# Optimization experiments

Measured on AMD Instinct MI355X. Metric: run time of the kernel, lower is better.

## Reference

```python
import jax, jax.numpy as jnp
import numpy as np

B, S, D_MODEL, N_HEADS = 2, 2048, 2048, 16
HEAD_DIM = D_MODEL // N_HEADS
SCALE = 1.0 / np.sqrt(HEAD_DIM)
SOFTCAP = 30.0
NEG = -10000.0


def _apply_rope(h):
    # h: [B, S, H, D]; faithful to torch ref: repeat_interleave'd cos/sin with
    # half-split rotate_half.
    seq, d = h.shape[1], h.shape[3]
    pos = jnp.arange(seq, dtype=jnp.float32)
    inv_freq = 1.0 / (10000.0 ** (jnp.arange(0, d, 2, dtype=jnp.float32) / d))
    phase = pos[:, None] * inv_freq[None, :]                      # [S, D/2]
    cos = jnp.repeat(jnp.cos(phase), 2, axis=-1)[None, :, None, :].astype(h.dtype)
    sin = jnp.repeat(jnp.sin(phase), 2, axis=-1)[None, :, None, :].astype(h.dtype)
    rot = jnp.concatenate([-h[..., d // 2:], h[..., :d // 2]], axis=-1)
    return h * cos + rot * sin


def setup_inputs() -> dict:
    key = jax.random.key(0)
    k1, k2, k3, k4, k5 = jax.random.split(key, 5)
    hidden_states = jax.random.normal(k1, (B, S, D_MODEL), dtype=jnp.float32)
    # causal allowed-attention mask [S, S]; True = attention permitted
    allowed_attention = jnp.tril(jnp.ones((S, S), dtype=bool))
    # no padding (True would mean padded position)
    padding_mask = jnp.zeros((B, S), dtype=bool)
    std = 1.0 / np.sqrt(D_MODEL)
    Wq = jax.random.normal(k2, (D_MODEL, D_MODEL), dtype=jnp.float32) * std
    Wk = jax.random.normal(k3, (D_MODEL, D_MODEL), dtype=jnp.float32) * std
    Wv = jax.random.normal(k4, (D_MODEL, D_MODEL), dtype=jnp.float32) * std
    Wo = jax.random.normal(k5, (D_MODEL, D_MODEL), dtype=jnp.float32) * std
    return {"hidden_states": hidden_states, "allowed_attention": allowed_attention,
            "padding_mask": padding_mask, "Wq": Wq, "Wk": Wk, "Wv": Wv, "Wo": Wo}


def reference(hidden_states, allowed_attention, padding_mask, Wq, Wk, Wv, Wo):
    b, s, _ = hidden_states.shape
    q = (hidden_states @ Wq.T).reshape(b, s, N_HEADS, HEAD_DIM)
    k = (hidden_states @ Wk.T).reshape(b, s, N_HEADS, HEAD_DIM)
    v = (hidden_states @ Wv.T).reshape(b, s, N_HEADS, HEAD_DIM)
    q = _apply_rope(q)
    k = _apply_rope(k)
    logits = jnp.einsum('bthd,bshd->bhts', q, k).astype(jnp.float32) * SCALE
    logits = SOFTCAP * jnp.tanh(logits / SOFTCAP)
    logits = jnp.where(allowed_attention[None, None, :, :], logits, NEG)
    logits = jnp.where(padding_mask[:, None, None, :], NEG, logits)
    weights = jax.nn.softmax(logits, axis=-1).astype(q.dtype)
    attended = jnp.einsum('bhts,bshd->bthd', weights, v).reshape(b, s, D_MODEL)
    out = attended @ Wo.T
    return jnp.where(padding_mask[:, :, None], 0.0, out)
```

## Files before the change

kernel.cpp:

```cpp
#include <hip/hip_runtime.h>
#include <hip/hip_bf16.h>

#define S_LEN 2048
#define NH    16
#define HD    128
#define BHN   32
#define DM    2048
#define MTOK  4096
#define NTK   32

typedef __attribute__((ext_vector_type(8))) short short8;
typedef __attribute__((ext_vector_type(4))) float f32x4;

__device__ __forceinline__ unsigned short f2bf(float x){
  union { __hip_bfloat16 h; unsigned short u; } c; c.h = __float2bfloat16(x); return c.u;
}
__device__ __forceinline__ float bf2f(unsigned short u){
  union { unsigned short u; __hip_bfloat16 h; } c; c.u = u; return __bfloat162float(c.h);
}

__global__ void cvt_kernel(const float* __restrict__ src, unsigned short* __restrict__ dst, int n4){
  int i = blockIdx.x*256 + threadIdx.x;
  if (i >= n4) return;
  float4 v = reinterpret_cast<const float4*>(src)[i];
  ushort4 o;
  o.x = f2bf(v.x); o.y = f2bf(v.y); o.z = f2bf(v.z); o.w = f2bf(v.w);
  reinterpret_cast<ushort4*>(dst)[i] = o;
}

__global__ void cvt_w_kernel(const float* __restrict__ s0, const float* __restrict__ s1,
                             const float* __restrict__ s2, const float* __restrict__ s3,
                             unsigned short* __restrict__ dqkv, unsigned short* __restrict__ dwo,
                             int n4each){
  int which = blockIdx.y;
  const float* src = (which==0) ? s0 : (which==1) ? s1 : (which==2) ? s2 : s3;
  unsigned short* dst = (which<3) ? (dqkv + (size_t)which*DM*DM) : dwo;
  int i = blockIdx.x*256 + threadIdx.x;
  if (i >= n4each) return;
  float4 v = reinterpret_cast<const float4*>(src)[i];
  ushort4 o;
  o.x = f2bf(v.x); o.y = f2bf(v.y); o.z = f2bf(v.z); o.w = f2bf(v.w);
  reinterpret_cast<ushort4*>(dst)[i] = o;
}

__global__ void rope_table_kernel(float* __restrict__ cosT, float* __restrict__ sinT){
  int s = blockIdx.x, i = threadIdx.x;
  float inv = powf(10000.f, -(float)i * (1.f/64.f));
  float ph = (float)s * inv;
  float sv, cv; sincosf(ph, &sv, &cv);
  cosT[s*64 + i] = cv; sinT[s*64 + i] = sv;
}

__global__ void rope_apply2_kernel(unsigned short* __restrict__ Q, unsigned short* __restrict__ K,
                                   const float* __restrict__ cosT, const float* __restrict__ sinT){
  int gid = blockIdx.x*256 + threadIdx.x;
  unsigned short* X = (gid < (BHN*S_LEN*64)) ? Q : K;
  int g = gid & (BHN*S_LEN*64 - 1);
  int j = g & 63, row = g >> 6, s = row & (S_LEN-1);
  unsigned short* p = X + (size_t)row*HD;
  float h0 = bf2f(p[j]), h1 = bf2f(p[j+64]);
  int f0 = j >> 1;
  float c0 = cosT[s*64+f0],    s0 = sinT[s*64+f0];
  float c1 = cosT[s*64+32+f0], s1 = sinT[s*64+32+f0];
  p[j]    = f2bf(h0*c0 - h1*s0);
  p[j+64] = f2bf(h1*c1 + h0*s1);
}

#define MFMA8(ACC) \
  __builtin_amdgcn_s_setprio(1); \
  _Pragma("unroll") \
  for (int mi=0;mi<4;++mi){ \
    ACC[mi] = __builtin_amdgcn_mfma_f32_16x16x32_bf16(af[mi*2+0], bf[0], ACC[mi], 0,0,0); \
    ACC[mi] = __builtin_amdgcn_mfma_f32_16x16x32_bf16(af[mi*2+1], bf[1], ACC[mi], 0,0,0); \
  } \
  __builtin_amdgcn_s_setprio(0);

template<int MODE>
__global__ __launch_bounds__(512)
void gemm_8p(const unsigned short* __restrict__ A, const unsigned short* __restrict__ B,
             float* __restrict__ C0, unsigned short* __restrict__ Cq,
             unsigned short* __restrict__ Ck, unsigned short* __restrict__ Cv){
  extern __shared__ unsigned char sm[];
  const int t = threadIdx.x;
  const int lane = t & 63, w = t >> 6;
  const int lr = lane & 15, lg = lane >> 4;
  const int wm = w >> 2, wn = w & 3;
  int id = blockIdx.x, bm, bn;
  if (MODE == 3){ int swz = (id & 7)*96 + (id >> 3); bm = swz/48; bn = swz%48; }
  else          { int swz = (id & 7)*32 + (id >> 3); bm = swz/16; bn = swz%16; }
  const size_t rs = 4096;
  const unsigned char* Ab = (const unsigned char*)A + (size_t)bm*256*rs;
  const unsigned char* Bb = (const unsigned char*)B + (size_t)bn*128*rs;
  const int r0 = t >> 3, c0 = t & 7;

  auto stage = [&](int tkt, int slot){
    if (tkt >= NTK) return;
    unsigned char* hb = sm + ((tkt & 1) ? 49152 : 0);
    if (slot < 2){
      const unsigned char* sb = Ab + (size_t)(slot ? 128 : 0)*rs + (size_t)tkt*128;
      hb += slot*16384;
      __builtin_amdgcn_global_load_lds(
          (const unsigned int*)(sb + (size_t)r0*rs + ((unsigned)(c0 ^ (r0 & 7)) << 4)),
          (unsigned int*)(hb + t*16), 16, 0, 0);
      int r1 = r0 + 64;
      __builtin_amdgcn_global_load_lds(
          (const unsigned int*)(sb + (size_t)r1*rs + ((unsigned)(c0 ^ (r1 & 7)) << 4)),
          (unsigned int*)(hb + 8192 + t*16), 16, 0, 0);
    } else {
      const unsigned char* sb = Bb + (size_t)((slot-2) ? 64 : 0)*rs + (size_t)tkt*128;
      hb += 32768 + (slot-2)*8192;
      __builtin_amdgcn_global_load_lds(
          (const unsigned int*)(sb + (size_t)r0*rs + ((unsigned)(c0 ^ (r0 & 7)) << 4)),
          (unsigned int*)(hb + t*16), 16, 0, 0);
    }
  };

  short8 af[8], bf[2];
  auto loadA = [&](int d, int rh){
#pragma unroll
    for (int mi=0;mi<4;++mi){
      int row = wm*64 + mi*16 + lr;
      const unsigned char* rp = sm + d*49152 + rh*16384 + row*128;
      int x = row & 7;
      af[mi*2+0] = *reinterpret_cast<const short8*>(rp + (((0+lg) ^ x) << 4));
      af[mi*2+1] = *reinterpret_cast<const short8*>(rp + (((4+lg) ^ x) << 4));
    }
  };
  auto loadB = [&](int d, int ch){
    int row = wn*16 + lr;
    const unsigned char* rp = sm + d*49152 + 32768 + ch*8192 + row*128;
    int x = row & 7;
    bf[0] = *reinterpret_cast<const short8*>(rp + (((0+lg) ^ x) << 4));
    bf[1] = *reinterpret_cast<const short8*>(rp + (((4+lg) ^ x) << 4));
  };

  f32x4 acc00[4] = {}, acc01[4] = {}, acc11[4] = {}, acc10[4] = {};

  stage(0,0); stage(0,2); stage(0,3); stage(0,1);
  stage(1,0); stage(1,3); stage(1,1);
  asm volatile("s_waitcnt vmcnt(5)" ::: "memory");
  __builtin_amdgcn_s_barrier();

  for (int g = 0; g < NTK; ++g){
    const int d = g & 1;
    loadA(d, 0); loadB(d, 0);
    stage(g+1, 2);
    __builtin_amdgcn_s_barrier();
    MFMA8(acc00);
    __builtin_amdgcn_s_barrier();
    loadB(d, 1);
    stage(g+2, 0);
    __builtin_amdgcn_s_barrier();
    MFMA8(acc01);
    __builtin_amdgcn_s_barrier();
    loadA(d, 1);
    stage(g+2, 3);
    __builtin_amdgcn_s_barrier();
    MFMA8(acc11);
    __builtin_amdgcn_s_barrier();
    loadB(d, 0);
    stage(g+2, 1);
    __builtin_amdgcn_s_barrier();
    MFMA8(acc10);
    if (g < NTK-1){
      if (g == NTK-2) { asm volatile("s_waitcnt vmcnt(0)" ::: "memory"); }
      else            { asm volatile("s_waitcnt vmcnt(5)" ::: "memory"); }
    }
    __builtin_amdgcn_s_barrier();
  }

  auto epi = [&](const f32x4* acc, int rh, int ch){
#pragma unroll
    for (int mi=0;mi<4;++mi){
      int col  = bn*128 + ch*64 + wn*16 + lr;
      int rowb = bm*256 + rh*128 + wm*64 + mi*16 + lg*4;
      if (MODE == 0){
#pragma unroll
        for (int rr=0;rr<4;++rr)
          C0[(size_t)(rowb+rr)*DM + col] = acc[mi][rr];
      } else {
        if (col < 4096){
          unsigned short* dst = (col < 2048) ? Cq : Ck;
          int cc = col & 2047, h = cc >> 7, dd = cc & 127;
#pragma unroll
          for (int rr=0;rr<4;++rr){
            int row = rowb + rr, bb = row >> 11, s = row & 2047;
            dst[(((size_t)(bb*16+h)*2048 + s)<<7) + dd] = f2bf(acc[mi][rr]);
          }
        } else {
          int cc = col - 4096, h = cc >> 7, dd = cc & 127;
          ushort4 pk;
          pk.x = f2bf(acc[mi][0]); pk.y = f2bf(acc[mi][1]);
          pk.z = f2bf(acc[mi][2]); pk.w = f2bf(acc[mi][3]);
          int bb = rowb >> 11, s = rowb & 2047, kb = s >> 6, kvl = s & 63;
          *reinterpret_cast<ushort4*>(&Cv[(((size_t)((bb*16+h)*32 + kb)*128 + dd)<<6) + kvl]) = pk;
        }
      }
    }
  };
  epi(acc00,0,0); epi(acc01,0,1); epi(acc11,1,1); epi(acc10,1,0);
}

__global__ __launch_bounds__(256, 2)
void attn_kernel(const unsigned short* __restrict__ Qr, const unsigned short* __restrict__ Kr,
                 const unsigned short* __restrict__ Vp, unsigned short* __restrict__ AO){
  const int bid = blockIdx.x;
  const int qb  = (bid < 256) ? (15 - (bid >> 5)) : ((bid >> 5) - 8);
  const int bh  = bid & 31;
  const int t = threadIdx.x;
  const int w = t >> 6, lane = t & 63, lr = lane & 15, lg = lane >> 4;
  const int qbase = qb*128 + w*32;
  const int diag_w = (qbase + 31) >> 6;
  const int kmax = qb*2 + 1;
  const unsigned short* Qh = Qr + (size_t)bh*S_LEN*HD;
  const unsigned char*  Kg = (const unsigned char*)(Kr + (size_t)bh*S_LEN*HD);
  const unsigned char*  Vg = (const unsigned char*)Vp + (size_t)bh*32*16384;

  __shared__ __align__(16) unsigned short Ks[8192];
  __shared__ __align__(16) unsigned short Vs[8192];
  __shared__ __align__(16) unsigned short Ps[4][32][72];

  short8 qa[2][4];
#pragma unroll
  for (int f=0;f<2;++f)
#pragma unroll
    for (int kc=0;kc<4;++kc)
      qa[f][kc] = *reinterpret_cast<const short8*>(&Qh[(size_t)(qbase + f*16 + lr)*HD + kc*32 + lg*8]);

  float lsum[2] = {0.f, 0.f};
  f32x4 o[2][8] = {};

  const float C1 = 2.f * 0.08838834764831845f * 1.4426950408889634f / 30.f;
  const float C2 = -60.f * 1.4426950408889634f;

  for (int kb = 0; kb <= kmax; ++kb){
    const unsigned char* Kt = Kg + (size_t)kb*(64*256);
    const unsigned char* Vt = Vg + (size_t)kb*16384;
#pragma unroll
    for (int j=0;j<4;++j){
      unsigned int L  = (unsigned int)(w*4+j)*1024u + (unsigned int)lane*16u;
      unsigned int rK = L >> 8;
      unsigned int sK = (L & 255u) ^ ((rK & 15u) << 4);
      __builtin_amdgcn_global_load_lds((const unsigned int*)(Kt + (rK<<8) + sK),
          (unsigned int*)((unsigned char*)Ks + (size_t)(w*4+j)*1024), 16, 0, 0);
      unsigned int rV = L >> 7;
      unsigned int sV = (L & 127u) ^ ((rV & 7u) << 4);
      __builtin_amdgcn_global_load_lds((const unsigned int*)(Vt + (rV<<7) + sV),
          (unsigned int*)((unsigned char*)Vs + (size_t)(w*4+j)*1024), 16, 0, 0);
    }
    __syncthreads();
    if (kb <= diag_w){
      f32x4 s[2][4] = {};
      __builtin_amdgcn_s_setprio(1);
#pragma unroll
      for (int nf=0;nf<4;++nf)
#pragma unroll
        for (int kc=0;kc<4;++kc){
          unsigned int byt = ((unsigned int)(nf*16+lr) << 8) + (((unsigned int)(kc*64 + lg*16)) ^ ((unsigned int)(lr&15) << 4));
          short8 kf = *reinterpret_cast<const short8*>((const unsigned char*)Ks + byt);
          s[0][nf] = __builtin_amdgcn_mfma_f32_16x16x32_bf16(kf, qa[0][kc], s[0][nf], 0,0,0);
          s[1][nf] = __builtin_amdgcn_mfma_f32_16x16x32_bf16(kf, qa[1][kc], s[1][nf], 0,0,0);
        }
      __builtin_amdgcn_s_setprio(0);
#pragma unroll
      for (int f=0;f<2;++f){
#pragma unroll
        for (int nf=0;nf<4;++nf){
#pragma unroll
          for (int r=0;r<4;++r){
            float u = __builtin_amdgcn_exp2f(s[f][nf][r] * C1);
            float p = __builtin_amdgcn_exp2f(C2 * __builtin_amdgcn_rcpf(u + 1.f));
            if (kb == diag_w){
              int kvi = kb*64 + nf*16 + lg*4 + r;
              if (kvi > qbase + f*16 + lr) p = 0.f;
            }
            s[f][nf][r] = p;
            lsum[f] += p;
          }
          ushort4 pk;
          pk.x = f2bf(s[f][nf][0]); pk.y = f2bf(s[f][nf][1]);
          pk.z = f2bf(s[f][nf][2]); pk.w = f2bf(s[f][nf][3]);
          *reinterpret_cast<ushort4*>(&Ps[w][f*16+lr][nf*16 + lg*4]) = pk;
        }
      }
      short8 pb[2][2];
#pragma unroll
      for (int f=0;f<2;++f)
#pragma unroll
        for (int kc2=0;kc2<2;++kc2)
          pb[f][kc2] = *reinterpret_cast<const short8*>(&Ps[w][f*16+lr][kc2*32 + lg*8]);
      __builtin_amdgcn_s_setprio(1);
#pragma unroll
      for (int df=0;df<8;++df)
#pragma unroll
        for (int kc2=0;kc2<2;++kc2){
          unsigned int byt = ((unsigned int)(df*16+lr) << 7) + (((unsigned int)(kc2*64 + lg*16)) ^ ((unsigned int)(lr&7) << 4));
          short8 vb = *reinterpret_cast<const short8*>((const unsigned char*)Vs + byt);
          o[0][df] = __builtin_amdgcn_mfma_f32_16x16x32_bf16(vb, pb[0][kc2], o[0][df], 0,0,0);
          o[1][df] = __builtin_amdgcn_mfma_f32_16x16x32_bf16(vb, pb[1][kc2], o[1][df], 0,0,0);
        }
      __builtin_amdgcn_s_setprio(0);
    }
    __syncthreads();
  }
#pragma unroll
  for (int f=0;f<2;++f){
    lsum[f] += __shfl_xor(lsum[f], 16);
    lsum[f] += __shfl_xor(lsum[f], 32);
  }
  const int bb = bh >> 4, h = bh & 15;
#pragma unroll
  for (int f=0;f<2;++f){
    const float inv = 1.f / lsum[f];
    const int qi = qbase + f*16 + lr;
#pragma unroll
    for (int df=0;df<8;++df){
      ushort4 pk;
      pk.x = f2bf(o[f][df][0] * inv); pk.y = f2bf(o[f][df][1] * inv);
      pk.z = f2bf(o[f][df][2] * inv); pk.w = f2bf(o[f][df][3] * inv);
      *reinterpret_cast<ushort4*>(&AO[((size_t)(bb*S_LEN + qi))*DM + h*HD + df*16 + lg*4]) = pk;
    }
  }
}

extern "C" void kernel_launch(void* const* d_in, const int* in_sizes, int n_in,
                              void* d_out, int out_size, void* d_ws, size_t ws_size,
                              hipStream_t stream){
  const float* hs = (const float*)d_in[0];
  const float* Wq = (const float*)d_in[3];
  const float* Wk = (const float*)d_in[4];
  const float* Wv = (const float*)d_in[5];
  const float* Wo = (const float*)d_in[6];

  uint8_t* base = (uint8_t*)d_ws;
  unsigned short* hsb  = (unsigned short*)base; base += (size_t)MTOK*DM*2;
  unsigned short* wqkv = (unsigned short*)base; base += (size_t)3*DM*DM*2;
  unsigned short* wob  = (unsigned short*)base; base += (size_t)DM*DM*2;
  unsigned short* Qr   = (unsigned short*)base; base += (size_t)MTOK*DM*2;
  unsigned short* Kr   = (unsigned short*)base; base += (size_t)MTOK*DM*2;
  unsigned short* Vp   = (unsigned short*)base; base += (size_t)MTOK*DM*2;
  unsigned short* AO   = (unsigned short*)base; base += (size_t)MTOK*DM*2;
  float* cosT = (float*)base;                   base += (size_t)S_LEN*64*4;
  float* sinT = (float*)base;                   base += (size_t)S_LEN*64*4;

  cvt_kernel<<<(MTOK*DM/4)/256, 256, 0, stream>>>(hs, hsb, MTOK*DM/4);
  cvt_w_kernel<<<dim3((DM*DM/4)/256, 4), 256, 0, stream>>>(Wq, Wk, Wv, Wo, wqkv, wob, DM*DM/4);
  rope_table_kernel<<<S_LEN, 64, 0, stream>>>(cosT, sinT);

  hipFuncSetAttribute((const void*)gemm_8p<3>,
                      hipFuncAttributeMaxDynamicSharedMemorySize, 98304);
  hipFuncSetAttribute((const void*)gemm_8p<0>,
                      hipFuncAttributeMaxDynamicSharedMemorySize, 98304);

  gemm_8p<3><<<768, 512, 98304, stream>>>(hsb, wqkv, nullptr, Qr, Kr, Vp);

  rope_apply2_kernel<<<(2*BHN*S_LEN*64)/256, 256, 0, stream>>>(Qr, Kr, cosT, sinT);

  attn_kernel<<<512, 256, 0, stream>>>(Qr, Kr, Vp, AO);

  gemm_8p<0><<<256, 512, 98304, stream>>>(AO, wob, (float*)d_out, nullptr, nullptr, nullptr);
}
```

Before: 285.1 us.

## Replace 8-phase GEMM with two-phase double-buffered GEMM using wider N tiles

Replaces the 8-phase ping-pong GEMM (256x128 tiles, four sub-phase barriers per k-step) with a simpler two-phase loop. Each k-step prefetches the whole next tile into the other buffer, then runs all MFMAs for the current one. Tiles become 128x384 for the QKV projection (512 blocks, 128KB LDS) and 128x256 for the output projection. The block-to-tile mapping changes to a new swizzle. The aim is fewer barriers and more MFMA work per LDS fill, at the cost of a full vmcnt(0) wait each iteration, more registers for larger accumulators, and possibly lower occupancy.

After: 267.2 us. 1.07x faster.

```diff
diff --git a/kernel.cpp b/kernel.cpp
--- a/kernel.cpp
+++ b/kernel.cpp
@@ -66,118 +66,97 @@
   p[j+64] = f2bf(h1*c1 + h0*s1);
 }
 
-#define MFMA8(ACC) \
-  __builtin_amdgcn_s_setprio(1); \
-  _Pragma("unroll") \
-  for (int mi=0;mi<4;++mi){ \
-    ACC[mi] = __builtin_amdgcn_mfma_f32_16x16x32_bf16(af[mi*2+0], bf[0], ACC[mi], 0,0,0); \
-    ACC[mi] = __builtin_amdgcn_mfma_f32_16x16x32_bf16(af[mi*2+1], bf[1], ACC[mi], 0,0,0); \
-  } \
-  __builtin_amdgcn_s_setprio(0);
-
 template<int MODE>
 __global__ __launch_bounds__(512)
-void gemm_8p(const unsigned short* __restrict__ A, const unsigned short* __restrict__ B,
-             float* __restrict__ C0, unsigned short* __restrict__ Cq,
-             unsigned short* __restrict__ Ck, unsigned short* __restrict__ Cv){
+void gemm_2ph(const unsigned short* __restrict__ A, const unsigned short* __restrict__ B,
+              float* __restrict__ C0, unsigned short* __restrict__ Cq,
+              unsigned short* __restrict__ Ck, unsigned short* __restrict__ Cv){
+  constexpr int BN   = (MODE==3) ? 384 : 256;
+  constexpr int NJ   = BN/64;
+  constexpr int NBJ  = BN/64;
+  constexpr int BUFSZ = 16384 + BN*128;
   extern __shared__ unsigned char sm[];
   const int t = threadIdx.x;
   const int lane = t & 63, w = t >> 6;
   const int lr = lane & 15, lg = lane >> 4;
   const int wm = w >> 2, wn = w & 3;
-  int id = blockIdx.x, bm, bn;
-  if (MODE == 3){ int swz = (id & 7)*96 + (id >> 3); bm = swz/48; bn = swz%48; }
-  else          { int swz = (id & 7)*32 + (id >> 3); bm = swz/16; bn = swz%16; }
+  int bm, bn;
+  if (MODE == 3){ int x = blockIdx.x & 7, i = blockIdx.x >> 3;
+                  bn = x*2 + (i >> 5); bm = i & 31; }
+  else          { bn = blockIdx.x & 7; bm = blockIdx.x >> 3; }
   const size_t rs = 4096;
-  const unsigned char* Ab = (const unsigned char*)A + (size_t)bm*256*rs;
-  const unsigned char* Bb = (const unsigned char*)B + (size_t)bn*128*rs;
+  const unsigned char* Ab = (const unsigned char*)A + (size_t)bm*128*rs;
+  const unsigned char* Bb = (const unsigned char*)B + (size_t)bn*BN*rs;
   const int r0 = t >> 3, c0 = t & 7;
-
-  auto stage = [&](int tkt, int slot){
+  const int cs = (c0 ^ (r0 & 7)) << 4;
+
+  auto stage = [&](int tkt){
     if (tkt >= NTK) return;
-    unsigned char* hb = sm + ((tkt & 1) ? 49152 : 0);
-    if (slot < 2){
-      const unsigned char* sb = Ab + (size_t)(slot ? 128 : 0)*rs + (size_t)tkt*128;
-      hb += slot*16384;
-      __builtin_amdgcn_global_load_lds(
-          (const unsigned int*)(sb + (size_t)r0*rs + ((unsigned)(c0 ^ (r0 & 7)) << 4)),
-          (unsigned int*)(hb + t*16), 16, 0, 0);
-      int r1 = r0 + 64;
-      __builtin_amdgcn_global_load_lds(
-          (const unsigned int*)(sb + (size_t)r1*rs + ((unsigned)(c0 ^ (r1 & 7)) << 4)),
-          (unsigned int*)(hb + 8192 + t*16), 16, 0, 0);
-    } else {
-      const unsigned char* sb = Bb + (size_t)((slot-2) ? 64 : 0)*rs + (size_t)tkt*128;
-      hb += 32768 + (slot-2)*8192;
-      __builtin_amdgcn_global_load_lds(
-          (const unsigned int*)(sb + (size_t)r0*rs + ((unsigned)(c0 ^ (r0 & 7)) << 4)),
-          (unsigned int*)(hb + t*16), 16, 0, 0);
-    }
+    unsigned char* hb = sm + (tkt & 1)*BUFSZ;
+    const unsigned char* At = Ab + (size_t)tkt*128;
+    __builtin_amdgcn_global_load_lds((const unsigned int*)(At + (size_t)r0*rs + cs),
+        (unsigned int*)(hb + t*16), 16, 0, 0);
+    __builtin_amdgcn_global_load_lds((const unsigned int*)(At + (size_t)(r0+64)*rs + cs),
+        (unsigned int*)(hb + 8192 + t*16), 16, 0, 0);
+    const unsigned char* Bt = Bb + (size_t)tkt*128;
+#pragma unroll
+    for (int j=0;j<NBJ;++j)
+      __builtin_amdgcn_global_load_lds((const unsigned int*)(Bt + (size_t)(r0+64*j)*rs + cs),
+          (unsigned int*)(hb + 16384 + (size_t)(t + 512*j)*16), 16, 0, 0);
   };
 
-  short8 af[8], bf[2];
-  auto loadA = [&](int d, int rh){
+  f32x4 acc[4][NJ] = {};
+
+  stage(0);
+  asm volatile("s_waitcnt vmcnt(0)" ::: "memory");
+  __builtin_amdgcn_s_barrier();
+
+  for (int g = 0; g < NTK; ++g){
+    stage(g+1);
+    const unsigned char* hb = sm + (g & 1)*BUFSZ;
+    short8 af[8];
 #pragma unroll
     for (int mi=0;mi<4;++mi){
       int row = wm*64 + mi*16 + lr;
-      const unsigned char* rp = sm + d*49152 + rh*16384 + row*128;
-      int x = row & 7;
-      af[mi*2+0] = *reinterpret_cast<const short8*>(rp + (((0+lg) ^ x) << 4));
-      af[mi*2+1] = *reinterpret_cast<const short8*>(rp + (((4+lg) ^ x) << 4));
-    }
-  };
-  auto loadB = [&](int d, int ch){
-    int row = wn*16 + lr;
-    const unsigned char* rp = sm + d*49152 + 32768 + ch*8192 + row*128;
-    int x = row & 7;
-    bf[0] = *reinterpret_cast<const short8*>(rp + (((0+lg) ^ x) << 4));
-    bf[1] = *reinterpret_cast<const short8*>(rp + (((4+lg) ^ x) << 4));
-  };
-
-  f32x4 acc00[4] = {}, acc01[4] = {}, acc11[4] = {}, acc10[4] = {};
-
-  stage(0,0); stage(0,2); stage(0,3); stage(0,1);
-  stage(1,0); stage(1,3); stage(1,1);
-  asm volatile("s_waitcnt vmcnt(5)" ::: "memory");
-  __builtin_amdgcn_s_barrier();
-
-  for (int g = 0; g < NTK; ++g){
-    const int d = g & 1;
-    loadA(d, 0); loadB(d, 0);
-    stage(g+1, 2);
-    __builtin_amdgcn_s_barrier();
-    MFMA8(acc00);
-    __builtin_amdgcn_s_barrier();
-    loadB(d, 1);
-    stage(g+2, 0);
-    __builtin_amdgcn_s_barrier();
-    MFMA8(acc01);
-    __builtin_amdgcn_s_barrier();
-    loadA(d, 1);
-    stage(g+2, 3);
-    __builtin_amdgcn_s_barrier();
-    MFMA8(acc11);
-    __builtin_amdgcn_s_barrier();
-    loadB(d, 0);
-    stage(g+2, 1);
-    __builtin_amdgcn_s_barrier();
-    MFMA8(acc10);
-    if (g < NTK-1){
-      if (g == NTK-2) { asm volatile("s_waitcnt vmcnt(0)" ::: "memory"); }
-      else            { asm volatile("s_waitcnt vmcnt(5)" ::: "memory"); }
-    }
+      const unsigned char* rp = hb + row*128;
+      int x = (row & 7) << 4;
+#pragma unroll
+      for (int ks=0;ks<2;++ks)
+        af[mi*2+ks] = *reinterpret_cast<const short8*>(rp + (((ks*4+lg) << 4) ^ x));
+    }
+    short8 bfr[NJ*2];
+#pragma unroll
+    for (int nj=0;nj<NJ;++nj){
+      int row = wn*(BN/4) + nj*16 + lr;
+      const unsigned char* rp = hb + 16384 + row*128;
+      int x = (row & 7) << 4;
+#pragma unroll
+      for (int ks=0;ks<2;++ks)
+        bfr[nj*2+ks] = *reinterpret_cast<const short8*>(rp + (((ks*4+lg) << 4) ^ x));
+    }
+    __builtin_amdgcn_s_setprio(1);
+#pragma unroll
+    for (int mi=0;mi<4;++mi)
+#pragma unroll
+      for (int nj=0;nj<NJ;++nj){
+        acc[mi][nj] = __builtin_amdgcn_mfma_f32_16x16x32_bf16(af[mi*2+0], bfr[nj*2+0], acc[mi][nj], 0,0,0);
+        acc[mi][nj] = __builtin_amdgcn_mfma_f32_16x16x32_bf16(af[mi*2+1], bfr[nj*2+1], acc[mi][nj], 0,0,0);
+      }
+    __builtin_amdgcn_s_setprio(0);
+    asm volatile("s_waitcnt vmcnt(0)" ::: "memory");
     __builtin_amdgcn_s_barrier();
   }
 
-  auto epi = [&](const f32x4* acc, int rh, int ch){
-#pragma unroll
-    for (int mi=0;mi<4;++mi){
-      int col  = bn*128 + ch*64 + wn*16 + lr;
-      int rowb = bm*256 + rh*128 + wm*64 + mi*16 + lg*4;
+#pragma unroll
+  for (int mi=0;mi<4;++mi)
+#pragma unroll
+    for (int nj=0;nj<NJ;++nj){
+      int col  = bn*BN + wn*(BN/4) + nj*16 + lr;
+      int rowb = bm*128 + wm*64 + mi*16 + lg*4;
       if (MODE == 0){
 #pragma unroll
         for (int rr=0;rr<4;++rr)
-          C0[(size_t)(rowb+rr)*DM + col] = acc[mi][rr];
+          C0[(size_t)(rowb+rr)*DM + col] = acc[mi][nj][rr];
       } else {
         if (col < 4096){
           unsigned short* dst = (col < 2048) ? Cq : Ck;
@@ -185,20 +164,18 @@
 #pragma unroll
           for (int rr=0;rr<4;++rr){
             int row = rowb + rr, bb = row >> 11, s = row & 2047;
-            dst[(((size_t)(bb*16+h)*2048 + s)<<7) + dd] = f2bf(acc[mi][rr]);
+            dst[(((size_t)(bb*16+h)*2048 + s)<<7) + dd] = f2bf(acc[mi][nj][rr]);
           }
         } else {
           int cc = col - 4096, h = cc >> 7, dd = cc & 127;
           ushort4 pk;
-          pk.x = f2bf(acc[mi][0]); pk.y = f2bf(acc[mi][1]);
-          pk.z = f2bf(acc[mi][2]); pk.w = f2bf(acc[mi][3]);
+          pk.x = f2bf(acc[mi][nj][0]); pk.y = f2bf(acc[mi][nj][1]);
+          pk.z = f2bf(acc[mi][nj][2]); pk.w = f2bf(acc[mi][nj][3]);
           int bb = rowb >> 11, s = rowb & 2047, kb = s >> 6, kvl = s & 63;
           *reinterpret_cast<ushort4*>(&Cv[(((size_t)((bb*16+h)*32 + kb)*128 + dd)<<6) + kvl]) = pk;
         }
       }
     }
-  };
-  epi(acc00,0,0); epi(acc01,0,1); epi(acc11,1,1); epi(acc10,1,0);
 }
 
 __global__ __launch_bounds__(256, 2)
@@ -347,16 +324,16 @@
   cvt_w_kernel<<<dim3((DM*DM/4)/256, 4), 256, 0, stream>>>(Wq, Wk, Wv, Wo, wqkv, wob, DM*DM/4);
   rope_table_kernel<<<S_LEN, 64, 0, stream>>>(cosT, sinT);
 
-  hipFuncSetAttribute((const void*)gemm_8p<3>,
+  hipFuncSetAttribute((const void*)gemm_2ph<3>,
+                      hipFuncAttributeMaxDynamicSharedMemorySize, 131072);
+  hipFuncSetAttribute((const void*)gemm_2ph<0>,
                       hipFuncAttributeMaxDynamicSharedMemorySize, 98304);
-  hipFuncSetAttribute((const void*)gemm_8p<0>,
-                      hipFuncAttributeMaxDynamicSharedMemorySize, 98304);
-
-  gemm_8p<3><<<768, 512, 98304, stream>>>(hsb, wqkv, nullptr, Qr, Kr, Vp);
+
+  gemm_2ph<3><<<512, 512, 131072, stream>>>(hsb, wqkv, nullptr, Qr, Kr, Vp);
 
   rope_apply2_kernel<<<(2*BHN*S_LEN*64)/256, 256, 0, stream>>>(Qr, Kr, cosT, sinT);
 
   attn_kernel<<<512, 256, 0, stream>>>(Qr, Kr, Vp, AO);
 
-  gemm_8p<0><<<256, 512, 98304, stream>>>(AO, wob, (float*)d_out, nullptr, nullptr, nullptr);
-}
+  gemm_2ph<0><<<256, 512, 98304, stream>>>(AO, wob, (float*)d_out, nullptr, nullptr, nullptr);
+}
```
